# Kernel tuning notes

Hardware: AMD Instinct MI355X
Metric: run time of the kernel (lower is better)

The kernel has to match this reference:

```python
import jax, jax.numpy as jnp
import numpy as np

N, M, D = 2048, 2048, 16
H_INIT = 0.85


def setup_inputs() -> dict:
    key = jax.random.key(0)
    k1, k2 = jax.random.split(key)
    x = jax.random.normal(k1, (N, D), dtype=jnp.float32)
    X2 = jax.random.normal(k2, (M, D), dtype=jnp.float32)
    # log_H chosen so that softplus(log_H) == H_INIT, matching tf.Variable init
    log_H = jnp.asarray(np.log(np.exp(H_INIT) - 1.0), dtype=jnp.float32)
    return {"x": x, "X2": X2, "log_H": log_H}


def reference(x, X2, log_H):
    # fractional Brownian motion kernel:
    # K[i,j] = 0.5 * sum_d (|x_id|^2H + |X2_jd|^2H - |x_id - X2_jd|^2H)
    H = jax.nn.softplus(log_H)
    p = 2.0 * H
    # per-point terms do not depend on the other index -> sum over D first
    t1 = jnp.sum(jnp.abs(x) ** p, axis=-1)   # [N]
    t2 = jnp.sum(jnp.abs(X2) ** p, axis=-1)  # [M]
    # pairwise term: [N, M, D] broadcast, reduced over D
    t3 = jnp.sum(jnp.abs(x[:, None, :] - X2[None, :, :]) ** p, axis=-1)  # [N, M]
    K = 0.5 * (t1[:, None] + t2[None, :] - t3)
    return K
```

## Files before the change

### kernel.cpp

```cpp
#include <hip/hip_runtime.h>
#include <math.h>


#define D_DIM 16
#define BLK 64

__device__ __forceinline__ float powp(float t, float p) {
    return __builtin_amdgcn_exp2f(p * __builtin_amdgcn_logf(t));
}

__global__ __launch_bounds__(256) void fbm_kernel(
    const float* __restrict__ x,
    const float* __restrict__ X2,
    const float* __restrict__ logH,
    float* __restrict__ out,
    int N, int M)
{
    __shared__ float xs[D_DIM][BLK];
    __shared__ float ys[D_DIM][BLK];
    __shared__ float t1s[BLK];
    __shared__ float t2s[BLK];

    const int tid  = threadIdx.x;
    const int brow = blockIdx.y * BLK;
    const int bcol = blockIdx.x * BLK;

    const float p = 2.0f * log1pf(expf(logH[0]));

    {
        float4 vx = ((const float4*)(x  + (size_t)brow * D_DIM))[tid];
        float4 vy = ((const float4*)(X2 + (size_t)bcol * D_DIM))[tid];
        int r  = tid >> 2;
        int d0 = (tid & 3) << 2;
        xs[d0 + 0][r] = vx.x; xs[d0 + 1][r] = vx.y;
        xs[d0 + 2][r] = vx.z; xs[d0 + 3][r] = vx.w;
        ys[d0 + 0][r] = vy.x; ys[d0 + 1][r] = vy.y;
        ys[d0 + 2][r] = vy.z; ys[d0 + 3][r] = vy.w;
    }
    __syncthreads();

    if (tid < 128) {
        int r = tid & 63;
        const float (*src)[BLK] = (tid < 64) ? xs : ys;
        float s = 0.0f;
        #pragma unroll
        for (int d = 0; d < D_DIM; ++d) {
            s += powp(fabsf(src[d][r]), p);
        }
        if (tid < 64) t1s[r] = s; else t2s[r] = s;
    }
    __syncthreads();

    const int ti = tid >> 4;
    const int tj = tid & 15;

    float acc[4][4] = {};

    #pragma unroll
    for (int d = 0; d < D_DIM; ++d) {
        float4 xa = *(const float4*)&xs[d][ti * 4];
        float4 xb = *(const float4*)&ys[d][tj * 4];
        float a0 = xa.x, a1 = xa.y, a2 = xa.z, a3 = xa.w;
        float b0 = xb.x, b1 = xb.y, b2 = xb.z, b3 = xb.w;

        acc[0][0] += powp(fabsf(a0 - b0), p);
        acc[0][1] += powp(fabsf(a0 - b1), p);
        acc[0][2] += powp(fabsf(a0 - b2), p);
        acc[0][3] += powp(fabsf(a0 - b3), p);
        acc[1][0] += powp(fabsf(a1 - b0), p);
        acc[1][1] += powp(fabsf(a1 - b1), p);
        acc[1][2] += powp(fabsf(a1 - b2), p);
        acc[1][3] += powp(fabsf(a1 - b3), p);
        acc[2][0] += powp(fabsf(a2 - b0), p);
        acc[2][1] += powp(fabsf(a2 - b1), p);
        acc[2][2] += powp(fabsf(a2 - b2), p);
        acc[2][3] += powp(fabsf(a2 - b3), p);
        acc[3][0] += powp(fabsf(a3 - b0), p);
        acc[3][1] += powp(fabsf(a3 - b1), p);
        acc[3][2] += powp(fabsf(a3 - b2), p);
        acc[3][3] += powp(fabsf(a3 - b3), p);
    }

    float t2v0 = t2s[tj * 4 + 0];
    float t2v1 = t2s[tj * 4 + 1];
    float t2v2 = t2s[tj * 4 + 2];
    float t2v3 = t2s[tj * 4 + 3];

    #pragma unroll
    for (int a = 0; a < 4; ++a) {
        float t1v = t1s[ti * 4 + a];
        float4 o;
        o.x = 0.5f * (t1v + t2v0 - acc[a][0]);
        o.y = 0.5f * (t1v + t2v1 - acc[a][1]);
        o.z = 0.5f * (t1v + t2v2 - acc[a][2]);
        o.w = 0.5f * (t1v + t2v3 - acc[a][3]);
        int gi = brow + ti * 4 + a;
        *(float4*)(out + (size_t)gi * M + bcol + tj * 4) = o;
    }
}

extern "C" void kernel_launch(void* const* d_in, const int* in_sizes, int n_in,
                              void* d_out, int out_size, void* d_ws, size_t ws_size,
                              hipStream_t stream) {
    const float* x    = (const float*)d_in[0];
    const float* X2   = (const float*)d_in[1];
    const float* logH = (const float*)d_in[2];
    float* out = (float*)d_out;

    int N = in_sizes[0] / D_DIM;
    int M = in_sizes[1] / D_DIM;

    dim3 grid(M / BLK, N / BLK);
    dim3 block(256);
    fbm_kernel<<<grid, block, 0, stream>>>(x, X2, logH, out, N, M);
}
```

Measured before the change: 22.16 us.

## Replace transcendental pow with mantissa polynomial and exponent lookup table

Computes |d|^(2H) as (d^2)^H by splitting the float's bits: a degree-4 polynomial in the mantissa fitted at runtime to m^H on [1,2], times a shared-memory table of 2^(H*(e-127)) indexed by the exponent. This swaps the per-element log2/exp2 transcendental pair for FMAs plus an LDS lookup. The polynomial is an approximation, so accuracy depends on the fit, and the table reads add LDS traffic and possible bank conflicts.

Result: slower. 26.52 us (+19.7%).

```diff
diff --git a/kernel.cpp b/kernel.cpp
--- a/kernel.cpp
+++ b/kernel.cpp
@@ -5,8 +5,8 @@
 #define D_DIM 16
 #define BLK 64
 
-__device__ __forceinline__ float powp(float t, float p) {
-    return __builtin_amdgcn_exp2f(p * __builtin_amdgcn_logf(t));
+__device__ __forceinline__ float powH(float v, float H) {
+    return __builtin_amdgcn_exp2f(H * __builtin_amdgcn_logf(v));
 }
 
 __global__ __launch_bounds__(256) void fbm_kernel(
@@ -16,6 +16,7 @@
     float* __restrict__ out,
     int N, int M)
 {
+    __shared__ float tbl[256];
     __shared__ float xs[D_DIM][BLK];
     __shared__ float ys[D_DIM][BLK];
     __shared__ float t1s[BLK];
@@ -25,7 +26,31 @@
     const int brow = blockIdx.y * BLK;
     const int bcol = blockIdx.x * BLK;
 
-    const float p = 2.0f * log1pf(expf(logH[0]));
+    const float H = log1pf(expf(logH[0]));
+
+    const float T1 = 0.475528258f, T2 = 0.293892626f;
+    float f0 = powH(1.5f + T1, H);
+    float f1 = powH(1.5f + T2, H);
+    float f2 = powH(1.5f,      H);
+    float f3 = powH(1.5f - T2, H);
+    float f4 = powH(1.5f - T1, H);
+    float s1 = 0.5f * (f0 + f4), d1 = 0.5f * (f0 - f4);
+    float s2 = 0.5f * (f1 + f3), d2 = 0.5f * (f1 - f3);
+    float u1 = T1 * T1, u2 = T2 * T2;
+    float A = s1 - f2, B = s2 - f2;
+    float det = u1 * u2 * (u2 - u1);
+    float e1 = (A * u2 * u2 - B * u1 * u1) / det;
+    float e2 = (B * u1 - A * u2) / det;
+    float Ap = d1 / T1, Bp = d2 / T2;
+    float o1 = (Ap - Bp) / (u1 - u2);
+    float o0 = Ap - o1 * u1;
+    float a4 = e2;
+    float a3 = o1 - 6.0f * e2;
+    float a2 = e1 - 4.5f * o1 + 13.5f * e2;
+    float a1 = o0 - 3.0f * e1 + 6.75f * o1 - 13.5f * e2;
+    float a0 = f2 - 1.5f * o0 + 2.25f * e1 - 3.375f * o1 + 5.0625f * e2;
+
+    tbl[tid & 255] = __builtin_amdgcn_exp2f(H * ((float)(tid & 255) - 127.0f));
 
     {
         float4 vx = ((const float4*)(x  + (size_t)brow * D_DIM))[tid];
@@ -39,13 +64,21 @@
     }
     __syncthreads();
 
+    #define POWP(S_) ({ \
+        unsigned bits_ = __float_as_uint(S_); \
+        float m_ = __uint_as_float((bits_ & 0x007FFFFFu) | 0x3F800000u); \
+        float g_ = fmaf(fmaf(fmaf(fmaf(a4, m_, a3), m_, a2), m_, a1), m_, a0); \
+        g_ * tbl[bits_ >> 23]; })
+
     if (tid < 128) {
         int r = tid & 63;
         const float (*src)[BLK] = (tid < 64) ? xs : ys;
         float s = 0.0f;
         #pragma unroll
         for (int d = 0; d < D_DIM; ++d) {
-            s += powp(fabsf(src[d][r]), p);
+            float v = src[d][r];
+            float sq = fmaf(v, v, 1e-30f);
+            s += POWP(sq);
         }
         if (tid < 64) t1s[r] = s; else t2s[r] = s;
     }
@@ -56,30 +89,27 @@
 
     float acc[4][4] = {};
 
+    #define TERM(A_, B_, R_, C_) { \
+        float u_ = (A_) - (B_); \
+        float s_ = fmaf(u_, u_, 1e-30f); \
+        unsigned bits_ = __float_as_uint(s_); \
+        float m_ = __uint_as_float((bits_ & 0x007FFFFFu) | 0x3F800000u); \
+        float g_ = fmaf(fmaf(fmaf(fmaf(a4, m_, a3), m_, a2), m_, a1), m_, a0); \
+        acc[R_][C_] = fmaf(g_, tbl[bits_ >> 23], acc[R_][C_]); }
+
     #pragma unroll
     for (int d = 0; d < D_DIM; ++d) {
         float4 xa = *(const float4*)&xs[d][ti * 4];
         float4 xb = *(const float4*)&ys[d][tj * 4];
-        float a0 = xa.x, a1 = xa.y, a2 = xa.z, a3 = xa.w;
-        float b0 = xb.x, b1 = xb.y, b2 = xb.z, b3 = xb.w;
+        float A0 = xa.x, A1 = xa.y, A2 = xa.z, A3 = xa.w;
+        float B0 = xb.x, B1 = xb.y, B2 = xb.z, B3 = xb.w;
 
-        acc[0][0] += powp(fabsf(a0 - b0), p);
-        acc[0][1] += powp(fabsf(a0 - b1), p);
-        acc[0][2] += powp(fabsf(a0 - b2), p);
-        acc[0][3] += powp(fabsf(a0 - b3), p);
-        acc[1][0] += powp(fabsf(a1 - b0), p);
-        acc[1][1] += powp(fabsf(a1 - b1), p);
-        acc[1][2] += powp(fabsf(a1 - b2), p);
-        acc[1][3] += powp(fabsf(a1 - b3), p);
-        acc[2][0] += powp(fabsf(a2 - b0), p);
-        acc[2][1] += powp(fabsf(a2 - b1), p);
-        acc[2][2] += powp(fabsf(a2 - b2), p);
-        acc[2][3] += powp(fabsf(a2 - b3), p);
-        acc[3][0] += powp(fabsf(a3 - b0), p);
-        acc[3][1] += powp(fabsf(a3 - b1), p);
-        acc[3][2] += powp(fabsf(a3 - b2), p);
-        acc[3][3] += powp(fabsf(a3 - b3), p);
+        TERM(A0, B0, 0, 0) TERM(A0, B1, 0, 1) TERM(A0, B2, 0, 2) TERM(A0, B3, 0, 3)
+        TERM(A1, B0, 1, 0) TERM(A1, B1, 1, 1) TERM(A1, B2, 1, 2) TERM(A1, B3, 1, 3)
+        TERM(A2, B0, 2, 0) TERM(A2, B1, 2, 1) TERM(A2, B2, 2, 2) TERM(A2, B3, 2, 3)
+        TERM(A3, B0, 3, 0) TERM(A3, B1, 3, 1) TERM(A3, B2, 3, 2) TERM(A3, B3, 3, 3)
     }
+    #undef TERM
 
     float t2v0 = t2s[tj * 4 + 0];
     float t2v1 = t2s[tj * 4 + 1];
```
